# Optimization experiments

Measured on AMD Instinct MI355X. Metric: run time of the kernel, lower is better.

The kernel has to match this reference:

```python
import jax, jax.numpy as jnp
import numpy as np

EPS = 1e-5

def setup_inputs() -> dict:
    key = jax.random.key(0)
    ks = jax.random.split(key, 10)
    B, C, H, W, D = 1, 128, 20, 20, 20
    Cq = C // 8
    s = 0.05
    return {
        "x":   jax.random.normal(ks[0], (B, C, H, W, D), jnp.float32),
        "wq":  jax.random.normal(ks[1], (Cq, C), jnp.float32) * s,
        "bq":  jnp.zeros((Cq,), jnp.float32),
        "wk":  jax.random.normal(ks[2], (Cq, C), jnp.float32) * s,
        "bk":  jnp.zeros((Cq,), jnp.float32),
        "wv":  jax.random.normal(ks[3], (C, C), jnp.float32) * s,
        "bv":  jnp.zeros((C,), jnp.float32),
        "wa":  jax.random.normal(ks[4], (C, C), jnp.float32) * s,
        "ba":  jnp.zeros((C,), jnp.float32),
        "bn_w": jnp.ones((C,), jnp.float32),
        "bn_b": jnp.zeros((C,), jnp.float32),
    }

def reference(x, wq, bq, wk, bk, wv, bv, wa, ba, bn_w, bn_b):
    B, C, H, W, D = x.shape
    N = H * W * D
    xf = x.reshape(B, C, N)                                   # (B,C,N)
    # 1x1 conv projections = per-position channel matmuls
    q = jnp.einsum('oc,bcn->bno', wq, xf) + bq                # (B,N,Cq)
    k = jnp.einsum('oc,bcn->bon', wk, xf) + bk[:, None]       # (B,Cq,N)
    v = jnp.einsum('oc,bcn->bon', wv, xf) + bv[:, None]       # (B,C,N)
    # raw (unscaled) attention, softmax over key positions
    att = jax.nn.softmax(jnp.einsum('bnc,bcm->bnm', q, k), axis=-1)  # (B,N,N)
    # att_value[b,c,i] = sum_j value[b,c,j] * att[b,i,j]
    av = jnp.einsum('bcj,bij->bci', v, att)                   # (B,C,N)
    y = jnp.einsum('oc,bcn->bon', wa, av) + ba[:, None]       # (B,C,N)
    # BatchNorm (training mode): per-channel stats over batch + spatial
    mean = jnp.mean(y, axis=(0, 2), keepdims=True)
    var = jnp.var(y, axis=(0, 2), keepdims=True)
    y = (y - mean) * jax.lax.rsqrt(var + EPS) * bn_w[:, None] + bn_b[:, None]
    out = jax.nn.relu(y) + xf
    return out.reshape(B, C, H, W, D)
```

## Files before the change

kernel.cpp:

```cpp
#include <hip/hip_runtime.h>
#include <math.h>

#define N_POS 8000
#define C_CH  128
#define KSPLIT 5
#define KT_PER 25

typedef __bf16 bf16x8 __attribute__((ext_vector_type(8)));
typedef float  f32x4  __attribute__((ext_vector_type(4)));

#define MFMA(a,b,c) __builtin_amdgcn_mfma_f32_16x16x32_bf16((a),(b),(c),0,0,0)


#define GLOAD_LDS(gp, lp) \
    __builtin_amdgcn_global_load_lds( \
        (const __attribute__((address_space(1))) void*)(gp), \
        (__attribute__((address_space(3))) void*)(lp), 16, 0, 0)

__global__ __launch_bounds__(256) void qkv_kernel(
    const float* __restrict__ x,
    const float* __restrict__ wq, const float* __restrict__ bq,
    const float* __restrict__ wk, const float* __restrict__ bk,
    const float* __restrict__ wv, const float* __restrict__ bv,
    __bf16* __restrict__ q_bf, __bf16* __restrict__ k_bf, __bf16* __restrict__ v_bf)
{
    __shared__ __bf16 x_lds[32 * 136];
    __shared__ __bf16 v_out[128 * 36];

    const int t    = threadIdx.x;
    const int n0   = blockIdx.x * 32;
    const int lane = t & 63;
    const int w    = t >> 6;
    const int l15  = lane & 15;
    const int quad = lane >> 4;

    for (int r = 0; r < 4; ++r) {
        int f = r * 256 + t;
        int ch = f >> 3, n4 = f & 7;
        float4 xv = *reinterpret_cast<const float4*>(&x[ch * N_POS + n0 + n4 * 4]);
        x_lds[(n4 * 4 + 0) * 136 + ch] = (__bf16)xv.x;
        x_lds[(n4 * 4 + 1) * 136 + ch] = (__bf16)xv.y;
        x_lds[(n4 * 4 + 2) * 136 + ch] = (__bf16)xv.z;
        x_lds[(n4 * 4 + 3) * 136 + ch] = (__bf16)xv.w;
    }

    bf16x8 aw[3][4];
    f32x4  acc[3][2];
    const int nmt = (w < 2) ? 3 : 2;
    for (int mi = 0; mi < nmt; ++mi) {
        int mt = w + 4 * mi;
        const float *wrow, *brow;
        if (mt == 0)      { wrow = wq + l15 * 128;               brow = bq; }
        else if (mt == 1) { wrow = wk + l15 * 128;               brow = bk; }
        else              { wrow = wv + ((mt - 2) * 16 + l15) * 128;
                            brow = bv + (mt - 2) * 16; }
        for (int ks = 0; ks < 4; ++ks) {
            float4 f0 = *reinterpret_cast<const float4*>(wrow + ks * 32 + quad * 8);
            float4 f1 = *reinterpret_cast<const float4*>(wrow + ks * 32 + quad * 8 + 4);
            bf16x8 a;
            a[0]=(__bf16)f0.x; a[1]=(__bf16)f0.y; a[2]=(__bf16)f0.z; a[3]=(__bf16)f0.w;
            a[4]=(__bf16)f1.x; a[5]=(__bf16)f1.y; a[6]=(__bf16)f1.z; a[7]=(__bf16)f1.w;
            aw[mi][ks] = a;
        }
        for (int ni = 0; ni < 2; ++ni) {
            acc[mi][ni][0] = brow[quad * 4 + 0]; acc[mi][ni][1] = brow[quad * 4 + 1];
            acc[mi][ni][2] = brow[quad * 4 + 2]; acc[mi][ni][3] = brow[quad * 4 + 3];
        }
    }
    __syncthreads();

    for (int ks = 0; ks < 4; ++ks) {
        bf16x8 b0 = *reinterpret_cast<const bf16x8*>(&x_lds[(0  + l15) * 136 + ks * 32 + quad * 8]);
        bf16x8 b1 = *reinterpret_cast<const bf16x8*>(&x_lds[(16 + l15) * 136 + ks * 32 + quad * 8]);
        for (int mi = 0; mi < nmt; ++mi) {
            acc[mi][0] = MFMA(aw[mi][ks], b0, acc[mi][0]);
            acc[mi][1] = MFMA(aw[mi][ks], b1, acc[mi][1]);
        }
    }

    union S4 { short4 s; __bf16 b[4]; };
    for (int mi = 0; mi < nmt; ++mi) {
        int mt = w + 4 * mi;
        for (int ni = 0; ni < 2; ++ni) {
            S4 u;
            u.b[0]=(__bf16)acc[mi][ni][0]; u.b[1]=(__bf16)acc[mi][ni][1];
            u.b[2]=(__bf16)acc[mi][ni][2]; u.b[3]=(__bf16)acc[mi][ni][3];
            int n = n0 + ni * 16 + l15;
            if (mt == 0) {
                *reinterpret_cast<short4*>(&q_bf[n * 16 + quad * 4]) = u.s;
            } else if (mt == 1) {
                *reinterpret_cast<short4*>(&k_bf[n * 16 + quad * 4]) = u.s;
            } else {
                int ch0 = (mt - 2) * 16 + quad * 4;
                int nl  = ni * 16 + l15;
                v_out[(ch0 + 0) * 36 + nl] = u.b[0];
                v_out[(ch0 + 1) * 36 + nl] = u.b[1];
                v_out[(ch0 + 2) * 36 + nl] = u.b[2];
                v_out[(ch0 + 3) * 36 + nl] = u.b[3];
            }
        }
    }
    __syncthreads();
    for (int r = 0; r < 4; ++r) {
        int f = r * 256 + t;
        int ch = f >> 3, n4 = f & 7;
        int2 d = *reinterpret_cast<const int2*>(&v_out[ch * 36 + n4 * 4]);
        *reinterpret_cast<int2*>(&v_bf[ch * N_POS + n0 + n4 * 4]) = d;
    }
}

__global__ __launch_bounds__(256, 4) void attn_kernel(
    const __bf16* __restrict__ q_bf, const __bf16* __restrict__ k_bf,
    const __bf16* __restrict__ v_bf, float* __restrict__ av_part,
    float* __restrict__ l_part)
{
    __shared__ __bf16 v_buf[2][8192];
    __shared__ __bf16 k_buf[2][1024];
    __shared__ __bf16 p_lds[2048];

    const int t    = threadIdx.x;
    const int qt   = blockIdx.x % 250;
    const int sp   = blockIdx.x / 250;
    const int n0q  = qt * 32;
    const int lane = t & 63;
    const int w    = t >> 6;
    const int l15  = lane & 15;
    const int quad = lane >> 4;

    const int chL   = lane >> 3;
    const int vpart = (lane & 7) ^ chL;
    const int kkey  = lane >> 1;
    const int khalf = lane & 1;

    bf16x8 aq[2];
    for (int ni = 0; ni < 2; ++ni) {
        for (int j = 0; j < 8; ++j) aq[ni][j] = (__bf16)0.0f;
        if (quad < 2)
            aq[ni] = *reinterpret_cast<const bf16x8*>(
                &q_bf[(n0q + ni * 16 + l15) * 16 + quad * 8]);
    }
    bf16x8 ones;
    for (int j = 0; j < 8; ++j) ones[j] = (__bf16)1.0f;

    f32x4 acc[2][2];
    for (int mi = 0; mi < 2; ++mi)
        for (int ni = 0; ni < 2; ++ni)
            for (int r = 0; r < 4; ++r) acc[mi][ni][r] = 0.f;
    f32x4 lacc[2];
    for (int ni = 0; ni < 2; ++ni)
        for (int r = 0; r < 4; ++r) lacc[ni][r] = 0.f;

    const int kt0 = kt0 < 0 ? 0 : sp * KT_PER;

    auto stage = [&](int kt, int buf) {
        const int n0k = kt * 64;
        for (int r = 0; r < 4; ++r) {
            int R = w * 4 + r;
            GLOAD_LDS(v_bf + (8 * R + chL) * N_POS + n0k + vpart * 8,
                      &v_buf[buf][R * 512]);
        }
        for (int h = 0; h < 2; ++h) {
            GLOAD_LDS(k_bf + (size_t)(n0k + h * 32 + kkey) * 16 + khalf * 8,
                      &k_buf[buf][h * 512]);
        }
    };

    stage(kt0, 0);

    const int oS  = w * 2 + (quad >> 1);
    const int sub = (quad & 1) * 4;

    for (int kt = kt0; kt < kt0 + KT_PER; ++kt) {
        const int cur = (kt - kt0) & 1;
        __syncthreads();

        bf16x8 ak;
        for (int j = 0; j < 8; ++j) ak[j] = (__bf16)0.0f;
        if (quad < 2)
            ak = *reinterpret_cast<const bf16x8*>(
                &k_buf[cur][(w * 16 + l15) * 16 + quad * 8]);
        f32x4 s0, s1;
        for (int r = 0; r < 4; ++r) { s0[r] = 0.f; s1[r] = 0.f; }
        s0 = MFMA(ak, aq[0], s0);
        s1 = MFMA(ak, aq[1], s1);
        union S4 { short4 sh; __bf16 b[4]; };
        {
            S4 u;
            u.b[0] = (__bf16)__expf(s0[0]); u.b[1] = (__bf16)__expf(s0[1]);
            u.b[2] = (__bf16)__expf(s0[2]); u.b[3] = (__bf16)__expf(s0[3]);
            *reinterpret_cast<short4*>(&p_lds[(oS * 32 + l15) * 8 + sub]) = u.sh;
            u.b[0] = (__bf16)__expf(s1[0]); u.b[1] = (__bf16)__expf(s1[1]);
            u.b[2] = (__bf16)__expf(s1[2]); u.b[3] = (__bf16)__expf(s1[3]);
            *reinterpret_cast<short4*>(&p_lds[(oS * 32 + 16 + l15) * 8 + sub]) = u.sh;
        }
        __syncthreads();

        if (kt + 1 < kt0 + KT_PER) stage(kt + 1, cur ^ 1);

        const int chl = l15 & 7;
        for (int ks = 0; ks < 2; ++ks) {
            int pz = ((ks * 4 + quad) ^ chl);
            bf16x8 a0 = *reinterpret_cast<const bf16x8*>(
                &v_buf[cur][(((2 * w)     * 2 + (l15 >> 3)) * 64 + chl * 8 + pz) * 8]);
            bf16x8 a1 = *reinterpret_cast<const bf16x8*>(
                &v_buf[cur][(((2 * w + 1) * 2 + (l15 >> 3)) * 64 + chl * 8 + pz) * 8]);
            bf16x8 p0 = *reinterpret_cast<const bf16x8*>(
                &p_lds[((ks * 4 + quad) * 32 + 0  + l15) * 8]);
            bf16x8 p1 = *reinterpret_cast<const bf16x8*>(
                &p_lds[((ks * 4 + quad) * 32 + 16 + l15) * 8]);
            acc[0][0] = MFMA(a0, p0, acc[0][0]);
            acc[0][1] = MFMA(a0, p1, acc[0][1]);
            acc[1][0] = MFMA(a1, p0, acc[1][0]);
            acc[1][1] = MFMA(a1, p1, acc[1][1]);
            if (w == 0) {
                lacc[0] = MFMA(ones, p0, lacc[0]);
                lacc[1] = MFMA(ones, p1, lacc[1]);
            }
        }
    }

    float* dst = av_part + (size_t)sp * 1024000;
    for (int mi = 0; mi < 2; ++mi)
        for (int ni = 0; ni < 2; ++ni) {
            int n  = n0q + ni * 16 + l15;
            int ch = (2 * w + mi) * 16 + quad * 4;
            *reinterpret_cast<f32x4*>(&dst[n * 128 + ch]) = acc[mi][ni];
        }
    if (w == 0 && quad == 0) {
        l_part[sp * N_POS + n0q + 0  + l15] = lacc[0][0];
        l_part[sp * N_POS + n0q + 16 + l15] = lacc[1][0];
    }
}

__global__ __launch_bounds__(256) void proj_out_kernel(
    const float* __restrict__ av_part, const float* __restrict__ l_part,
    const float* __restrict__ wa, const float* __restrict__ ba,
    float* __restrict__ y_ws, float* __restrict__ bn_sum, float* __restrict__ bn_sumsq)
{
    __shared__ __bf16 b_lds[4096];

    const int t    = threadIdx.x;
    const int n0   = blockIdx.x * 32;
    const int lane = t & 63;
    const int w    = t >> 6;
    const int l15  = lane & 15;
    const int quad = lane >> 4;

    for (int r = 0; r < 2; ++r) {
        int g = r * 256 + t;
        int n = g >> 4, oc = g & 15;
        float l = 0.f;
#pragma unroll
        for (int s = 0; s < KSPLIT; ++s) l += l_part[s * N_POS + n0 + n];
        float4 a0 = make_float4(0.f, 0.f, 0.f, 0.f);
        float4 a1 = make_float4(0.f, 0.f, 0.f, 0.f);
#pragma unroll
        for (int s = 0; s < KSPLIT; ++s) {
            const float* p = av_part + (size_t)s * 1024000 + (n0 + n) * 128 + oc * 8;
            float4 u = *reinterpret_cast<const float4*>(p);
            float4 v = *reinterpret_cast<const float4*>(p + 4);
            a0.x += u.x; a0.y += u.y; a0.z += u.z; a0.w += u.w;
            a1.x += v.x; a1.y += v.y; a1.z += v.z; a1.w += v.w;
        }
        float inv = 1.f / l;
        union { int4 iv; __bf16 b[8]; } u;
        u.b[0]=(__bf16)(a0.x*inv); u.b[1]=(__bf16)(a0.y*inv);
        u.b[2]=(__bf16)(a0.z*inv); u.b[3]=(__bf16)(a0.w*inv);
        u.b[4]=(__bf16)(a1.x*inv); u.b[5]=(__bf16)(a1.y*inv);
        u.b[6]=(__bf16)(a1.z*inv); u.b[7]=(__bf16)(a1.w*inv);
        int A = (n >> 4) * 16 + oc;
        int slot = (n & 15) ^ (oc & 7);
        *reinterpret_cast<int4*>(&b_lds[(A * 16 + slot) * 8]) = u.iv;
    }

    bf16x8 aw[2][4];
    f32x4  acc[2][2];
    for (int mi = 0; mi < 2; ++mi) {
        int mt = 2 * w + mi;
        const float* wrow = wa + (mt * 16 + l15) * 128;
        for (int ks = 0; ks < 4; ++ks) {
            float4 f0 = *reinterpret_cast<const float4*>(wrow + ks * 32 + quad * 8);
            float4 f1 = *reinterpret_cast<const float4*>(wrow + ks * 32 + quad * 8 + 4);
            bf16x8 a;
            a[0]=(__bf16)f0.x; a[1]=(__bf16)f0.y; a[2]=(__bf16)f0.z; a[3]=(__bf16)f0.w;
            a[4]=(__bf16)f1.x; a[5]=(__bf16)f1.y; a[6]=(__bf16)f1.z; a[7]=(__bf16)f1.w;
            aw[mi][ks] = a;
        }
        for (int ni = 0; ni < 2; ++ni) {
            acc[mi][ni][0] = ba[mt * 16 + quad * 4 + 0];
            acc[mi][ni][1] = ba[mt * 16 + quad * 4 + 1];
            acc[mi][ni][2] = ba[mt * 16 + quad * 4 + 2];
            acc[mi][ni][3] = ba[mt * 16 + quad * 4 + 3];
        }
    }
    __syncthreads();

    for (int ks = 0; ks < 4; ++ks) {
        int oc = ks * 4 + quad;
        int slot = l15 ^ (oc & 7);
        bf16x8 b0 = *reinterpret_cast<const bf16x8*>(&b_lds[((0  + oc) * 16 + slot) * 8]);
        bf16x8 b1 = *reinterpret_cast<const bf16x8*>(&b_lds[((16 + oc) * 16 + slot) * 8]);
        for (int mi = 0; mi < 2; ++mi) {
            acc[mi][0] = MFMA(aw[mi][ks], b0, acc[mi][0]);
            acc[mi][1] = MFMA(aw[mi][ks], b1, acc[mi][1]);
        }
    }

    for (int mi = 0; mi < 2; ++mi) {
        for (int r = 0; r < 4; ++r) {
            int ch = (2 * w + mi) * 16 + quad * 4 + r;
            float v0 = acc[mi][0][r];
            float v1 = acc[mi][1][r];
            y_ws[ch * N_POS + n0 + 0  + l15] = v0;
            y_ws[ch * N_POS + n0 + 16 + l15] = v1;
            float s1 = v0 + v1;
            float s2 = v0 * v0 + v1 * v1;
#pragma unroll
            for (int off = 8; off >= 1; off >>= 1) {
                s1 += __shfl_xor(s1, off, 64);
                s2 += __shfl_xor(s2, off, 64);
            }
            if (l15 == 0) {
                atomicAdd(&bn_sum[ch],   s1);
                atomicAdd(&bn_sumsq[ch], s2);
            }
        }
    }
}

__global__ __launch_bounds__(256) void bn_relu_kernel(
    const float* __restrict__ y_ws, const float* __restrict__ x,
    const float* __restrict__ bn_sum, const float* __restrict__ bn_sumsq,
    const float* __restrict__ bn_w, const float* __restrict__ bn_b,
    float* __restrict__ out)
{
    const int i4 = blockIdx.x * 256 + threadIdx.x;
    const int c  = i4 / 2000;
    const float mean  = bn_sum[c]   * (1.f / 8000.f);
    const float var   = bn_sumsq[c] * (1.f / 8000.f) - mean * mean;
    const float rstd  = rsqrtf(var + 1e-5f);
    const float scale = bn_w[c] * rstd;
    const float shift = bn_b[c] - mean * scale;

    float4 y4 = reinterpret_cast<const float4*>(y_ws)[i4];
    float4 x4 = reinterpret_cast<const float4*>(x)[i4];
    float4 o4;
    o4.x = fmaxf(y4.x * scale + shift, 0.f) + x4.x;
    o4.y = fmaxf(y4.y * scale + shift, 0.f) + x4.y;
    o4.z = fmaxf(y4.z * scale + shift, 0.f) + x4.z;
    o4.w = fmaxf(y4.w * scale + shift, 0.f) + x4.w;
    reinterpret_cast<float4*>(out)[i4] = o4;
}

extern "C" void kernel_launch(void* const* d_in, const int* in_sizes, int n_in,
                              void* d_out, int out_size, void* d_ws, size_t ws_size,
                              hipStream_t stream)
{
    const float* x    = (const float*)d_in[0];
    const float* wq   = (const float*)d_in[1];
    const float* bq   = (const float*)d_in[2];
    const float* wk   = (const float*)d_in[3];
    const float* bk   = (const float*)d_in[4];
    const float* wv   = (const float*)d_in[5];
    const float* bv   = (const float*)d_in[6];
    const float* wa   = (const float*)d_in[7];
    const float* ba   = (const float*)d_in[8];
    const float* bn_w = (const float*)d_in[9];
    const float* bn_b = (const float*)d_in[10];
    float* out = (float*)d_out;

    char* base = (char*)d_ws;
    float*  av_part = (float*)base;
    __bf16* q_bf    = (__bf16*)(base + 20480000);
    __bf16* k_bf    = (__bf16*)(base + 20736000);
    __bf16* v_bf    = (__bf16*)(base + 20992000);
    float*  l_part  = (float*)(base + 23040000);
    float*  bn_sum   = (float*)(base + 23200000);
    float*  bn_sumsq = bn_sum + 128;
    float*  y_ws    = (float*)(base + 23201024);

    hipMemsetAsync(bn_sum, 0, 1024, stream);
    qkv_kernel<<<250, 256, 0, stream>>>(x, wq, bq, wk, bk, wv, bv, q_bf, k_bf, v_bf);
    attn_kernel<<<250 * KSPLIT, 256, 0, stream>>>(q_bf, k_bf, v_bf, av_part, l_part);
    proj_out_kernel<<<250, 256, 0, stream>>>(av_part, l_part, wa, ba, y_ws, bn_sum, bn_sumsq);
    bn_relu_kernel<<<1000, 256, 0, stream>>>(y_ws, x, bn_sum, bn_sumsq, bn_w, bn_b, out);
}
```

Baseline: 177.4 us.

## Retile attention to 64 queries per block with register-prefetched K/V, bf16 partials

The attention kernel now handles 64 queries per block instead of 32 and drops the LDS staging of K/V through async global-to-LDS loads. Each wave instead loads its V and K fragments straight into registers, prefetched one tile ahead, which doubles reuse of each loaded K/V tile. Split-K partial outputs are stored as bf16 instead of fp32, halving partial traffic at some precision cost. The qkv and proj_out kernels shrink to 16 positions per block with more blocks. The BN stat zeroing moves from a memset into qkv_kernel, which removes one launch.

```diff
diff --git a/kernel.cpp b/kernel.cpp
--- a/kernel.cpp
+++ b/kernel.cpp
@@ -11,41 +11,40 @@
 
 #define MFMA(a,b,c) __builtin_amdgcn_mfma_f32_16x16x32_bf16((a),(b),(c),0,0,0)
 
-
-#define GLOAD_LDS(gp, lp) \
-    __builtin_amdgcn_global_load_lds( \
-        (const __attribute__((address_space(1))) void*)(gp), \
-        (__attribute__((address_space(3))) void*)(lp), 16, 0, 0)
 
 __global__ __launch_bounds__(256) void qkv_kernel(
     const float* __restrict__ x,
     const float* __restrict__ wq, const float* __restrict__ bq,
     const float* __restrict__ wk, const float* __restrict__ bk,
     const float* __restrict__ wv, const float* __restrict__ bv,
-    __bf16* __restrict__ q_bf, __bf16* __restrict__ k_bf, __bf16* __restrict__ v_bf)
-{
-    __shared__ __bf16 x_lds[32 * 136];
-    __shared__ __bf16 v_out[128 * 36];
+    __bf16* __restrict__ q_bf, __bf16* __restrict__ k_bf, __bf16* __restrict__ v_bf,
+    float* __restrict__ bn_stats)
+{
+    __shared__ __bf16 x_lds[2048];
+    __shared__ __bf16 v_out[2048];
 
     const int t    = threadIdx.x;
-    const int n0   = blockIdx.x * 32;
+    const int n0   = blockIdx.x * 16;
     const int lane = t & 63;
     const int w    = t >> 6;
     const int l15  = lane & 15;
     const int quad = lane >> 4;
 
-    for (int r = 0; r < 4; ++r) {
+    if (blockIdx.x == 0 && t < 256) bn_stats[t] = 0.f;
+
+    for (int r = 0; r < 2; ++r) {
         int f = r * 256 + t;
-        int ch = f >> 3, n4 = f & 7;
+        int ch = f >> 2, n4 = f & 3;
         float4 xv = *reinterpret_cast<const float4*>(&x[ch * N_POS + n0 + n4 * 4]);
-        x_lds[(n4 * 4 + 0) * 136 + ch] = (__bf16)xv.x;
-        x_lds[(n4 * 4 + 1) * 136 + ch] = (__bf16)xv.y;
-        x_lds[(n4 * 4 + 2) * 136 + ch] = (__bf16)xv.z;
-        x_lds[(n4 * 4 + 3) * 136 + ch] = (__bf16)xv.w;
+        int coct = ch >> 3, cl = ch & 7;
+        x_lds[((coct * 16 + n4 * 4 + 0) * 8) + cl] = (__bf16)xv.x;
+        x_lds[((coct * 16 + n4 * 4 + 1) * 8) + cl] = (__bf16)xv.y;
+        x_lds[((coct * 16 + n4 * 4 + 2) * 8) + cl] = (__bf16)xv.z;
+        x_lds[((coct * 16 + n4 * 4 + 3) * 8) + cl] = (__bf16)xv.w;
     }
 
     bf16x8 aw[3][4];
-    f32x4  acc[3][2];
+    f32x4  acc[3];
     const int nmt = (w < 2) ? 3 : 2;
     for (int mi = 0; mi < nmt; ++mi) {
         int mt = w + 4 * mi;
@@ -62,219 +61,190 @@
             a[4]=(__bf16)f1.x; a[5]=(__bf16)f1.y; a[6]=(__bf16)f1.z; a[7]=(__bf16)f1.w;
             aw[mi][ks] = a;
         }
-        for (int ni = 0; ni < 2; ++ni) {
-            acc[mi][ni][0] = brow[quad * 4 + 0]; acc[mi][ni][1] = brow[quad * 4 + 1];
-            acc[mi][ni][2] = brow[quad * 4 + 2]; acc[mi][ni][3] = brow[quad * 4 + 3];
-        }
+        acc[mi][0] = brow[quad * 4 + 0]; acc[mi][1] = brow[quad * 4 + 1];
+        acc[mi][2] = brow[quad * 4 + 2]; acc[mi][3] = brow[quad * 4 + 3];
     }
     __syncthreads();
 
     for (int ks = 0; ks < 4; ++ks) {
-        bf16x8 b0 = *reinterpret_cast<const bf16x8*>(&x_lds[(0  + l15) * 136 + ks * 32 + quad * 8]);
-        bf16x8 b1 = *reinterpret_cast<const bf16x8*>(&x_lds[(16 + l15) * 136 + ks * 32 + quad * 8]);
-        for (int mi = 0; mi < nmt; ++mi) {
-            acc[mi][0] = MFMA(aw[mi][ks], b0, acc[mi][0]);
-            acc[mi][1] = MFMA(aw[mi][ks], b1, acc[mi][1]);
-        }
+        bf16x8 b = *reinterpret_cast<const bf16x8*>(
+            &x_lds[((ks * 4 + quad) * 16 + l15) * 8]);
+        for (int mi = 0; mi < nmt; ++mi)
+            acc[mi] = MFMA(aw[mi][ks], b, acc[mi]);
     }
 
     union S4 { short4 s; __bf16 b[4]; };
     for (int mi = 0; mi < nmt; ++mi) {
         int mt = w + 4 * mi;
-        for (int ni = 0; ni < 2; ++ni) {
-            S4 u;
-            u.b[0]=(__bf16)acc[mi][ni][0]; u.b[1]=(__bf16)acc[mi][ni][1];
-            u.b[2]=(__bf16)acc[mi][ni][2]; u.b[3]=(__bf16)acc[mi][ni][3];
-            int n = n0 + ni * 16 + l15;
-            if (mt == 0) {
-                *reinterpret_cast<short4*>(&q_bf[n * 16 + quad * 4]) = u.s;
-            } else if (mt == 1) {
-                *reinterpret_cast<short4*>(&k_bf[n * 16 + quad * 4]) = u.s;
-            } else {
-                int ch0 = (mt - 2) * 16 + quad * 4;
-                int nl  = ni * 16 + l15;
-                v_out[(ch0 + 0) * 36 + nl] = u.b[0];
-                v_out[(ch0 + 1) * 36 + nl] = u.b[1];
-                v_out[(ch0 + 2) * 36 + nl] = u.b[2];
-                v_out[(ch0 + 3) * 36 + nl] = u.b[3];
-            }
+        S4 u;
+        u.b[0]=(__bf16)acc[mi][0]; u.b[1]=(__bf16)acc[mi][1];
+        u.b[2]=(__bf16)acc[mi][2]; u.b[3]=(__bf16)acc[mi][3];
+        int n = n0 + l15;
+        if (mt == 0) {
+            *reinterpret_cast<short4*>(&q_bf[n * 16 + quad * 4]) = u.s;
+        } else if (mt == 1) {
+            *reinterpret_cast<short4*>(&k_bf[n * 16 + quad * 4]) = u.s;
+        } else {
+            int ch0 = (mt - 2) * 16 + quad * 4;
+            v_out[(ch0 + 0) * 16 + l15] = u.b[0];
+            v_out[(ch0 + 1) * 16 + l15] = u.b[1];
+            v_out[(ch0 + 2) * 16 + l15] = u.b[2];
+            v_out[(ch0 + 3) * 16 + l15] = u.b[3];
         }
     }
     __syncthreads();
-    for (int r = 0; r < 4; ++r) {
-        int f = r * 256 + t;
-        int ch = f >> 3, n4 = f & 7;
-        int2 d = *reinterpret_cast<const int2*>(&v_out[ch * 36 + n4 * 4]);
-        *reinterpret_cast<int2*>(&v_bf[ch * N_POS + n0 + n4 * 4]) = d;
-    }
-}
-
-__global__ __launch_bounds__(256, 4) void attn_kernel(
+    {
+        int ch = t >> 1, half = t & 1;
+        int4 d = *reinterpret_cast<const int4*>(&v_out[ch * 16 + half * 8]);
+        *reinterpret_cast<int4*>(&v_bf[ch * N_POS + n0 + half * 8]) = d;
+    }
+}
+
+__global__ __launch_bounds__(256, 3) void attn_kernel(
     const __bf16* __restrict__ q_bf, const __bf16* __restrict__ k_bf,
-    const __bf16* __restrict__ v_bf, float* __restrict__ av_part,
+    const __bf16* __restrict__ v_bf, __bf16* __restrict__ av_part,
     float* __restrict__ l_part)
 {
-    __shared__ __bf16 v_buf[2][8192];
-    __shared__ __bf16 k_buf[2][1024];
-    __shared__ __bf16 p_lds[2048];
+    __shared__ __bf16 p_lds[4096];
 
     const int t    = threadIdx.x;
-    const int qt   = blockIdx.x % 250;
-    const int sp   = blockIdx.x / 250;
-    const int n0q  = qt * 32;
+    const int qt   = blockIdx.x % 125;
+    const int sp   = blockIdx.x / 125;
+    const int n0q  = qt * 64;
     const int lane = t & 63;
     const int w    = t >> 6;
     const int l15  = lane & 15;
     const int quad = lane >> 4;
 
-    const int chL   = lane >> 3;
-    const int vpart = (lane & 7) ^ chL;
-    const int kkey  = lane >> 1;
-    const int khalf = lane & 1;
-
-    bf16x8 aq[2];
-    for (int ni = 0; ni < 2; ++ni) {
-        for (int j = 0; j < 8; ++j) aq[ni][j] = (__bf16)0.0f;
+    bf16x8 aq[4];
+    for (int qh = 0; qh < 4; ++qh) {
+        for (int j = 0; j < 8; ++j) aq[qh][j] = (__bf16)0.0f;
         if (quad < 2)
-            aq[ni] = *reinterpret_cast<const bf16x8*>(
-                &q_bf[(n0q + ni * 16 + l15) * 16 + quad * 8]);
+            aq[qh] = *reinterpret_cast<const bf16x8*>(
+                &q_bf[(n0q + qh * 16 + l15) * 16 + quad * 8]);
     }
     bf16x8 ones;
     for (int j = 0; j < 8; ++j) ones[j] = (__bf16)1.0f;
 
-    f32x4 acc[2][2];
+    f32x4 acc[2][4];
     for (int mi = 0; mi < 2; ++mi)
-        for (int ni = 0; ni < 2; ++ni)
-            for (int r = 0; r < 4; ++r) acc[mi][ni][r] = 0.f;
-    f32x4 lacc[2];
-    for (int ni = 0; ni < 2; ++ni)
-        for (int r = 0; r < 4; ++r) lacc[ni][r] = 0.f;
-
-    const int kt0 = kt0 < 0 ? 0 : sp * KT_PER;
-
-    auto stage = [&](int kt, int buf) {
-        const int n0k = kt * 64;
-        for (int r = 0; r < 4; ++r) {
-            int R = w * 4 + r;
-            GLOAD_LDS(v_bf + (8 * R + chL) * N_POS + n0k + vpart * 8,
-                      &v_buf[buf][R * 512]);
-        }
-        for (int h = 0; h < 2; ++h) {
-            GLOAD_LDS(k_bf + (size_t)(n0k + h * 32 + kkey) * 16 + khalf * 8,
-                      &k_buf[buf][h * 512]);
-        }
-    };
-
-    stage(kt0, 0);
-
-    const int oS  = w * 2 + (quad >> 1);
-    const int sub = (quad & 1) * 4;
+        for (int qh = 0; qh < 4; ++qh)
+            for (int r = 0; r < 4; ++r) acc[mi][qh][r] = 0.f;
+    f32x4 lacc;
+    for (int r = 0; r < 4; ++r) lacc[r] = 0.f;
+
+    const int kt0 = sp * KT_PER;
+    const __bf16* vp0 = v_bf + (size_t)((2 * w)     * 16 + l15) * N_POS + kt0 * 64 + quad * 8;
+    const __bf16* vp1 = v_bf + (size_t)((2 * w + 1) * 16 + l15) * N_POS + kt0 * 64 + quad * 8;
+    const __bf16* kp  = k_bf + (size_t)(kt0 * 64 + w * 16 + l15) * 16 + quad * 8;
+
+    bf16x8 ak, a0[2], a1[2];
+    for (int j = 0; j < 8; ++j) ak[j] = (__bf16)0.0f;
+    if (quad < 2) ak = *reinterpret_cast<const bf16x8*>(kp);
+    for (int ks = 0; ks < 2; ++ks) {
+        a0[ks] = *reinterpret_cast<const bf16x8*>(vp0 + ks * 32);
+        a1[ks] = *reinterpret_cast<const bf16x8*>(vp1 + ks * 32);
+    }
+
+    const int pwc = (w * 2 + (quad >> 1)) * 16 + l15;
+    const int pwo = (quad & 1) * 4;
 
     for (int kt = kt0; kt < kt0 + KT_PER; ++kt) {
-        const int cur = (kt - kt0) & 1;
+        union S4 { short4 sh; __bf16 b[4]; };
+#pragma unroll
+        for (int qh = 0; qh < 4; ++qh) {
+            f32x4 s;
+            for (int r = 0; r < 4; ++r) s[r] = 0.f;
+            s = MFMA(ak, aq[qh], s);
+            S4 u;
+            u.b[0] = (__bf16)__expf(s[0]); u.b[1] = (__bf16)__expf(s[1]);
+            u.b[2] = (__bf16)__expf(s[2]); u.b[3] = (__bf16)__expf(s[3]);
+            *reinterpret_cast<short4*>(&p_lds[(qh * 128 + pwc) * 8 + pwo]) = u.sh;
+        }
         __syncthreads();
 
-        bf16x8 ak;
-        for (int j = 0; j < 8; ++j) ak[j] = (__bf16)0.0f;
-        if (quad < 2)
-            ak = *reinterpret_cast<const bf16x8*>(
-                &k_buf[cur][(w * 16 + l15) * 16 + quad * 8]);
-        f32x4 s0, s1;
-        for (int r = 0; r < 4; ++r) { s0[r] = 0.f; s1[r] = 0.f; }
-        s0 = MFMA(ak, aq[0], s0);
-        s1 = MFMA(ak, aq[1], s1);
-        union S4 { short4 sh; __bf16 b[4]; };
-        {
-            S4 u;
-            u.b[0] = (__bf16)__expf(s0[0]); u.b[1] = (__bf16)__expf(s0[1]);
-            u.b[2] = (__bf16)__expf(s0[2]); u.b[3] = (__bf16)__expf(s0[3]);
-            *reinterpret_cast<short4*>(&p_lds[(oS * 32 + l15) * 8 + sub]) = u.sh;
-            u.b[0] = (__bf16)__expf(s1[0]); u.b[1] = (__bf16)__expf(s1[1]);
-            u.b[2] = (__bf16)__expf(s1[2]); u.b[3] = (__bf16)__expf(s1[3]);
-            *reinterpret_cast<short4*>(&p_lds[(oS * 32 + 16 + l15) * 8 + sub]) = u.sh;
+        bf16x8 akN = ak, a0N[2], a1N[2];
+        a0N[0] = a0[0]; a0N[1] = a0[1]; a1N[0] = a1[0]; a1N[1] = a1[1];
+        if (kt + 1 < kt0 + KT_PER) {
+            if (quad < 2) akN = *reinterpret_cast<const bf16x8*>(kp + 64 * 16);
+            for (int ks = 0; ks < 2; ++ks) {
+                a0N[ks] = *reinterpret_cast<const bf16x8*>(vp0 + 64 + ks * 32);
+                a1N[ks] = *reinterpret_cast<const bf16x8*>(vp1 + 64 + ks * 32);
+            }
+        }
+
+#pragma unroll
+        for (int ks = 0; ks < 2; ++ks) {
+            bf16x8 p[4];
+#pragma unroll
+            for (int qh = 0; qh < 4; ++qh)
+                p[qh] = *reinterpret_cast<const bf16x8*>(
+                    &p_lds[((qh * 8 + ks * 4 + quad) * 16 + l15) * 8]);
+#pragma unroll
+            for (int qh = 0; qh < 4; ++qh) {
+                acc[0][qh] = MFMA(a0[ks], p[qh], acc[0][qh]);
+                acc[1][qh] = MFMA(a1[ks], p[qh], acc[1][qh]);
+            }
+            lacc = MFMA(ones, p[w], lacc);
         }
         __syncthreads();
 
-        if (kt + 1 < kt0 + KT_PER) stage(kt + 1, cur ^ 1);
-
-        const int chl = l15 & 7;
-        for (int ks = 0; ks < 2; ++ks) {
-            int pz = ((ks * 4 + quad) ^ chl);
-            bf16x8 a0 = *reinterpret_cast<const bf16x8*>(
-                &v_buf[cur][(((2 * w)     * 2 + (l15 >> 3)) * 64 + chl * 8 + pz) * 8]);
-            bf16x8 a1 = *reinterpret_cast<const bf16x8*>(
-                &v_buf[cur][(((2 * w + 1) * 2 + (l15 >> 3)) * 64 + chl * 8 + pz) * 8]);
-            bf16x8 p0 = *reinterpret_cast<const bf16x8*>(
-                &p_lds[((ks * 4 + quad) * 32 + 0  + l15) * 8]);
-            bf16x8 p1 = *reinterpret_cast<const bf16x8*>(
-                &p_lds[((ks * 4 + quad) * 32 + 16 + l15) * 8]);
-            acc[0][0] = MFMA(a0, p0, acc[0][0]);
-            acc[0][1] = MFMA(a0, p1, acc[0][1]);
-            acc[1][0] = MFMA(a1, p0, acc[1][0]);
-            acc[1][1] = MFMA(a1, p1, acc[1][1]);
-            if (w == 0) {
-                lacc[0] = MFMA(ones, p0, lacc[0]);
-                lacc[1] = MFMA(ones, p1, lacc[1]);
-            }
-        }
-    }
-
-    float* dst = av_part + (size_t)sp * 1024000;
+        ak = akN; a0[0] = a0N[0]; a0[1] = a0N[1]; a1[0] = a1N[0]; a1[1] = a1N[1];
+        kp += 64 * 16; vp0 += 64; vp1 += 64;
+    }
+
+    __bf16* dst = av_part + (size_t)sp * 1024000;
+    union S4o { short4 sh; __bf16 b[4]; };
     for (int mi = 0; mi < 2; ++mi)
-        for (int ni = 0; ni < 2; ++ni) {
-            int n  = n0q + ni * 16 + l15;
-            int ch = (2 * w + mi) * 16 + quad * 4;
-            *reinterpret_cast<f32x4*>(&dst[n * 128 + ch]) = acc[mi][ni];
-        }
-    if (w == 0 && quad == 0) {
-        l_part[sp * N_POS + n0q + 0  + l15] = lacc[0][0];
-        l_part[sp * N_POS + n0q + 16 + l15] = lacc[1][0];
-    }
+        for (int qh = 0; qh < 4; ++qh) {
+            S4o o;
+            o.b[0] = (__bf16)acc[mi][qh][0]; o.b[1] = (__bf16)acc[mi][qh][1];
+            o.b[2] = (__bf16)acc[mi][qh][2]; o.b[3] = (__bf16)acc[mi][qh][3];
+            *reinterpret_cast<short4*>(
+                &dst[(size_t)(n0q + qh * 16 + l15) * 128 + (2 * w + mi) * 16 + quad * 4]) = o.sh;
+        }
+    if (quad == 0)
+        l_part[sp * N_POS + n0q + w * 16 + l15] = lacc[0];
 }
 
 __global__ __launch_bounds__(256) void proj_out_kernel(
-    const float* __restrict__ av_part, const float* __restrict__ l_part,
+    const __bf16* __restrict__ av_part, const float* __restrict__ l_part,
     const float* __restrict__ wa, const float* __restrict__ ba,
     float* __restrict__ y_ws, float* __restrict__ bn_sum, float* __restrict__ bn_sumsq)
 {
-    __shared__ __bf16 b_lds[4096];
+    __shared__ __bf16 b_lds[2048];
 
     const int t    = threadIdx.x;
-    const int n0   = blockIdx.x * 32;
+    const int n0   = blockIdx.x * 16;
     const int lane = t & 63;
     const int w    = t >> 6;
     const int l15  = lane & 15;
     const int quad = lane >> 4;
 
-    for (int r = 0; r < 2; ++r) {
-        int g = r * 256 + t;
-        int n = g >> 4, oc = g & 15;
+    {
+        int n = t >> 4, oc = t & 15;
         float l = 0.f;
 #pragma unroll
         for (int s = 0; s < KSPLIT; ++s) l += l_part[s * N_POS + n0 + n];
-        float4 a0 = make_float4(0.f, 0.f, 0.f, 0.f);
-        float4 a1 = make_float4(0.f, 0.f, 0.f, 0.f);
+        float sum[8];
+#pragma unroll
+        for (int i = 0; i < 8; ++i) sum[i] = 0.f;
 #pragma unroll
         for (int s = 0; s < KSPLIT; ++s) {
-            const float* p = av_part + (size_t)s * 1024000 + (n0 + n) * 128 + oc * 8;
-            float4 u = *reinterpret_cast<const float4*>(p);
-            float4 v = *reinterpret_cast<const float4*>(p + 4);
-            a0.x += u.x; a0.y += u.y; a0.z += u.z; a0.w += u.w;
-            a1.x += v.x; a1.y += v.y; a1.z += v.z; a1.w += v.w;
+            bf16x8 p = *reinterpret_cast<const bf16x8*>(
+                &av_part[(size_t)s * 1024000 + (size_t)(n0 + n) * 128 + oc * 8]);
+#pragma unroll
+            for (int i = 0; i < 8; ++i) sum[i] += (float)p[i];
         }
         float inv = 1.f / l;
         union { int4 iv; __bf16 b[8]; } u;
-        u.b[0]=(__bf16)(a0.x*inv); u.b[1]=(__bf16)(a0.y*inv);
-        u.b[2]=(__bf16)(a0.z*inv); u.b[3]=(__bf16)(a0.w*inv);
-        u.b[4]=(__bf16)(a1.x*inv); u.b[5]=(__bf16)(a1.y*inv);
-        u.b[6]=(__bf16)(a1.z*inv); u.b[7]=(__bf16)(a1.w*inv);
-        int A = (n >> 4) * 16 + oc;
-        int slot = (n & 15) ^ (oc & 7);
-        *reinterpret_cast<int4*>(&b_lds[(A * 16 + slot) * 8]) = u.iv;
+#pragma unroll
+        for (int i = 0; i < 8; ++i) u.b[i] = (__bf16)(sum[i] * inv);
+        *reinterpret_cast<int4*>(&b_lds[(oc * 16 + n) * 8]) = u.iv;
     }
 
     bf16x8 aw[2][4];
-    f32x4  acc[2][2];
+    f32x4  acc[2];
     for (int mi = 0; mi < 2; ++mi) {
         int mt = 2 * w + mi;
         const float* wrow = wa + (mt * 16 + l15) * 128;
@@ -286,35 +256,27 @@
             a[4]=(__bf16)f1.x; a[5]=(__bf16)f1.y; a[6]=(__bf16)f1.z; a[7]=(__bf16)f1.w;
             aw[mi][ks] = a;
         }
-        for (int ni = 0; ni < 2; ++ni) {
-            acc[mi][ni][0] = ba[mt * 16 + quad * 4 + 0];
-            acc[mi][ni][1] = ba[mt * 16 + quad * 4 + 1];
-            acc[mi][ni][2] = ba[mt * 16 + quad * 4 + 2];
-            acc[mi][ni][3] = ba[mt * 16 + quad * 4 + 3];
-        }
+        acc[mi][0] = ba[mt * 16 + quad * 4 + 0];
+        acc[mi][1] = ba[mt * 16 + quad * 4 + 1];
+        acc[mi][2] = ba[mt * 16 + quad * 4 + 2];
+        acc[mi][3] = ba[mt * 16 + quad * 4 + 3];
     }
     __syncthreads();
 
     for (int ks = 0; ks < 4; ++ks) {
-        int oc = ks * 4 + quad;
-        int slot = l15 ^ (oc & 7);
-        bf16x8 b0 = *reinterpret_cast<const bf16x8*>(&b_lds[((0  + oc) * 16 + slot) * 8]);
-        bf16x8 b1 = *reinterpret_cast<const bf16x8*>(&b_lds[((16 + oc) * 16 + slot) * 8]);
-        for (int mi = 0; mi < 2; ++mi) {
-            acc[mi][0] = MFMA(aw[mi][ks], b0, acc[mi][0]);
-            acc[mi][1] = MFMA(aw[mi][ks], b1, acc[mi][1]);
-        }
+        bf16x8 b = *reinterpret_cast<const bf16x8*>(
+            &b_lds[((ks * 4 + quad) * 16 + l15) * 8]);
+        for (int mi = 0; mi < 2; ++mi)
+            acc[mi] = MFMA(aw[mi][ks], b, acc[mi]);
     }
 
     for (int mi = 0; mi < 2; ++mi) {
+#pragma unroll
         for (int r = 0; r < 4; ++r) {
             int ch = (2 * w + mi) * 16 + quad * 4 + r;
-            float v0 = acc[mi][0][r];
-            float v1 = acc[mi][1][r];
-            y_ws[ch * N_POS + n0 + 0  + l15] = v0;
-            y_ws[ch * N_POS + n0 + 16 + l15] = v1;
-            float s1 = v0 + v1;
-            float s2 = v0 * v0 + v1 * v1;
+            float v = acc[mi][r];
+            y_ws[ch * N_POS + n0 + l15] = v;
+            float s1 = v, s2 = v * v;
 #pragma unroll
             for (int off = 8; off >= 1; off >>= 1) {
                 s1 += __shfl_xor(s1, off, 64);
@@ -370,18 +332,18 @@
     float* out = (float*)d_out;
 
     char* base = (char*)d_ws;
-    float*  av_part = (float*)base;
-    __bf16* q_bf    = (__bf16*)(base + 20480000);
-    __bf16* k_bf    = (__bf16*)(base + 20736000);
-    __bf16* v_bf    = (__bf16*)(base + 20992000);
-    float*  l_part  = (float*)(base + 23040000);
-    float*  bn_sum   = (float*)(base + 23200000);
+    __bf16* av_part = (__bf16*)base;
+    __bf16* q_bf    = (__bf16*)(base + 10240000);
+    __bf16* k_bf    = (__bf16*)(base + 10496000);
+    __bf16* v_bf    = (__bf16*)(base + 10752000);
+    float*  l_part  = (float*)(base + 12800000);
+    float*  bn_sum   = (float*)(base + 12960000);
     float*  bn_sumsq = bn_sum + 128;
-    float*  y_ws    = (float*)(base + 23201024);
-
-    hipMemsetAsync(bn_sum, 0, 1024, stream);
-    qkv_kernel<<<250, 256, 0, stream>>>(x, wq, bq, wk, bk, wv, bv, q_bf, k_bf, v_bf);
-    attn_kernel<<<250 * KSPLIT, 256, 0, stream>>>(q_bf, k_bf, v_bf, av_part, l_part);
-    proj_out_kernel<<<250, 256, 0, stream>>>(av_part, l_part, wa, ba, y_ws, bn_sum, bn_sumsq);
+    float*  y_ws    = (float*)(base + 12961024);
+
+    qkv_kernel<<<500, 256, 0, stream>>>(x, wq, bq, wk, bk, wv, bv,
+                                        q_bf, k_bf, v_bf, bn_sum);
+    attn_kernel<<<125 * KSPLIT, 256, 0, stream>>>(q_bf, k_bf, v_bf, av_part, l_part);
+    proj_out_kernel<<<500, 256, 0, stream>>>(av_part, l_part, wa, ba, y_ws, bn_sum, bn_sumsq);
     bn_relu_kernel<<<1000, 256, 0, stream>>>(y_ws, x, bn_sum, bn_sumsq, bn_w, bn_b, out);
 }
```

Result: slower. 387.4 us (+118.4%).
